# Kernel optimization log

Measured on AMD Instinct MI355X. Metric: run time of the kernel, lower is better.

## Reference

```python
import jax, jax.numpy as jnp
import numpy as np

IO, H, S, N = 64, 1024, 512, 64

def setup_inputs() -> dict:
    key = jax.random.key(0)
    ks = jax.random.split(key, 6)
    scale = 0.05  # keep activations in a sane range for tanh/softmax
    return {
        "states": jax.random.normal(ks[0], (N, S, H), jnp.float32) * scale,
        "output_set": jax.random.normal(ks[1], (IO, H), jnp.float32) * scale,
        "Wo": jax.random.normal(ks[2], (2 * H, H), jnp.float32) * scale,
        "bo": jax.random.normal(ks[3], (H,), jnp.float32) * scale,
        "Wc": jax.random.normal(ks[4], (IO * H, IO), jnp.float32) * scale,
        "bc": jax.random.normal(ks[5], (IO,), jnp.float32) * scale,
    }

def reference(states, output_set, Wo, bo, Wc, bc):
    # Batched over the n_states Python loop of the original module.
    # attn scores: output_set [io,h] x states [n,s,h] -> [n,io,s]
    attn = jnp.einsum('ih,nsh->nis', output_set, states)
    attn = jax.nn.softmax(attn, axis=-1)  # softmax over context (sm_over_context=True)
    mix = jnp.einsum('nis,nsh->nih', attn, states)            # [n,io,h]
    out = jnp.broadcast_to(output_set[None], mix.shape)       # [n,io,h]
    combined = jnp.concatenate([mix, out], axis=-1)           # [n,io,2h]
    o = combined @ Wo + bo                                    # linear_out: 2h -> h
    logits = jnp.tanh(o).reshape(o.shape[0], -1) @ Wc + bc    # C: io*h -> io
    return logits
```

## Files before the change

### kernel.cpp

```cpp
#include <hip/hip_runtime.h>
#include <hip/hip_bf16.h>

#define IOdim 64
#define Hdim  1024
#define Sdim  512
#define Nbat  64

typedef __bf16 bf16x8_t __attribute__((ext_vector_type(8)));
typedef float  f32x4_t  __attribute__((ext_vector_type(4)));

#define MFMA16(a, b, c) __builtin_amdgcn_mfma_f32_16x16x32_bf16((a), (b), (c), 0, 0, 0)

__device__ __forceinline__ unsigned short f2bf(float f) {
    return __builtin_bit_cast(unsigned short, (__bf16)f);
}
__device__ __forceinline__ bf16x8_t cvt8(float4 p0, float4 p1) {
    bf16x8_t b;
    b[0] = (__bf16)p0.x; b[1] = (__bf16)p0.y; b[2] = (__bf16)p0.z; b[3] = (__bf16)p0.w;
    b[4] = (__bf16)p1.x; b[5] = (__bf16)p1.y; b[6] = (__bf16)p1.z; b[7] = (__bf16)p1.w;
    return b;
}

__global__ __launch_bounds__(256) void cvt_kernel(const float* __restrict__ in,
                                                  unsigned short* __restrict__ outp,
                                                  int nElem) {
    int idx = blockIdx.x * 256 + threadIdx.x;
    if (idx < nElem) outp[idx] = f2bf(in[idx]);
}

__global__ __launch_bounds__(256) void transpose_cvt(const float* __restrict__ in,
                                                     unsigned short* __restrict__ outp,
                                                     int R, int C) {
    __shared__ float tile[32][33];
    int c0 = blockIdx.x * 32, r0 = blockIdx.y * 32;
    int tx = threadIdx.x, ty = threadIdx.y;
#pragma unroll
    for (int i = 0; i < 4; i++) {
        int r = ty + i * 8;
        tile[r][tx] = in[(size_t)(r0 + r) * C + c0 + tx];
    }
    __syncthreads();
#pragma unroll
    for (int i = 0; i < 4; i++) {
        int r = ty + i * 8;
        outp[(size_t)(c0 + r) * R + r0 + tx] = f2bf(tile[tx][r]);
    }
}

__global__ __launch_bounds__(256) void scores_kernel(const float* __restrict__ states,
                                                     const unsigned short* __restrict__ osb,
                                                     float* __restrict__ attnf) {
    int n = blockIdx.y;
    int tid = threadIdx.x, lane = tid & 63, g = tid >> 6;
    int col = lane & 15, quad = lane >> 4;
    int s = blockIdx.x * 64 + g * 16 + col;
    const float* srow = states + (size_t)(n * Sdim + s) * Hdim + quad * 8;
    const unsigned short* ap = osb + (size_t)col * Hdim + quad * 8;
    f32x4_t acc0 = {0,0,0,0}, acc1 = {0,0,0,0}, acc2 = {0,0,0,0}, acc3 = {0,0,0,0};
    for (int kc = 0; kc < Hdim; kc += 32) {
        float4 p0 = *(const float4*)(srow + kc);
        float4 p1 = *(const float4*)(srow + kc + 4);
        bf16x8_t b  = cvt8(p0, p1);
        bf16x8_t a0 = *(const bf16x8_t*)(ap + kc);
        bf16x8_t a1 = *(const bf16x8_t*)(ap + 16 * Hdim + kc);
        bf16x8_t a2 = *(const bf16x8_t*)(ap + 32 * Hdim + kc);
        bf16x8_t a3 = *(const bf16x8_t*)(ap + 48 * Hdim + kc);
        acc0 = MFMA16(a0, b, acc0);
        acc1 = MFMA16(a1, b, acc1);
        acc2 = MFMA16(a2, b, acc2);
        acc3 = MFMA16(a3, b, acc3);
    }
    f32x4_t accs[4] = {acc0, acc1, acc2, acc3};
    float* ob = attnf + (size_t)(n * IOdim) * Sdim + blockIdx.x * 64 + g * 16 + col;
#pragma unroll
    for (int ai = 0; ai < 4; ai++)
#pragma unroll
        for (int r = 0; r < 4; r++) {
            int i = ai * 16 + quad * 4 + r;
            ob[i * Sdim] = accs[ai][r];
        }
}

__global__ __launch_bounds__(256) void softmax_kernel(const float* __restrict__ attnf,
                                                      unsigned short* __restrict__ attnb) {
    int row = blockIdx.x * 4 + (threadIdx.x >> 6);
    int lane = threadIdx.x & 63;
    const float* p = attnf + (size_t)row * Sdim + lane * 8;
    float4 v0 = ((const float4*)p)[0];
    float4 v1 = ((const float4*)p)[1];
    float v[8] = {v0.x, v0.y, v0.z, v0.w, v1.x, v1.y, v1.z, v1.w};
    float m = v[0];
#pragma unroll
    for (int j = 1; j < 8; j++) m = fmaxf(m, v[j]);
#pragma unroll
    for (int off = 32; off > 0; off >>= 1) m = fmaxf(m, __shfl_xor(m, off));
    float sum = 0.f;
#pragma unroll
    for (int j = 0; j < 8; j++) { v[j] = __expf(v[j] - m); sum += v[j]; }
#pragma unroll
    for (int off = 32; off > 0; off >>= 1) sum += __shfl_xor(sum, off);
    float inv = 1.0f / sum;
    union { unsigned short u[8]; uint4 q; } res;
#pragma unroll
    for (int j = 0; j < 8; j++) res.u[j] = f2bf(v[j] * inv);
    *(uint4*)(attnb + (size_t)row * Sdim + lane * 8) = res.q;
}

__global__ __launch_bounds__(256) void mix_kernel(const float* __restrict__ states,
                                                  const unsigned short* __restrict__ attnb,
                                                  unsigned short* __restrict__ mixb) {
    __shared__ unsigned short Tlds[64 * 72];
    int n = blockIdx.y, h0 = blockIdx.x * 64;
    int tid = threadIdx.x, lane = tid & 63, g = tid >> 6;
    int col = lane & 15, quad = lane >> 4;
    f32x4_t acc0 = {0,0,0,0}, acc1 = {0,0,0,0}, acc2 = {0,0,0,0}, acc3 = {0,0,0,0};
    const unsigned short* ap = attnb + (size_t)(n * IOdim + col) * Sdim + quad * 8;
    for (int sc = 0; sc < Sdim; sc += 64) {
        union { unsigned short u[16]; uint4 q[2]; } pk;
        const float* sp = states + (size_t)(n * Sdim + sc + g * 16) * Hdim + h0 + lane;
#pragma unroll
        for (int rep = 0; rep < 16; rep++) pk.u[rep] = f2bf(sp[(size_t)rep * Hdim]);
        if (sc) __syncthreads();
        *(uint4*)(Tlds + lane * 72 + g * 16)     = pk.q[0];
        *(uint4*)(Tlds + lane * 72 + g * 16 + 8) = pk.q[1];
        __syncthreads();
#pragma unroll
        for (int ks = 0; ks < 64; ks += 32) {
            bf16x8_t b  = *(const bf16x8_t*)(Tlds + (g * 16 + col) * 72 + ks + quad * 8);
            bf16x8_t a0 = *(const bf16x8_t*)(ap + sc + ks);
            bf16x8_t a1 = *(const bf16x8_t*)(ap + 16 * Sdim + sc + ks);
            bf16x8_t a2 = *(const bf16x8_t*)(ap + 32 * Sdim + sc + ks);
            bf16x8_t a3 = *(const bf16x8_t*)(ap + 48 * Sdim + sc + ks);
            acc0 = MFMA16(a0, b, acc0);
            acc1 = MFMA16(a1, b, acc1);
            acc2 = MFMA16(a2, b, acc2);
            acc3 = MFMA16(a3, b, acc3);
        }
    }
    f32x4_t accs[4] = {acc0, acc1, acc2, acc3};
    int h = h0 + g * 16 + col;
#pragma unroll
    for (int ai = 0; ai < 4; ai++)
#pragma unroll
        for (int r = 0; r < 4; r++) {
            int i = ai * 16 + quad * 4 + r;
            mixb[(size_t)(n * IOdim + i) * Hdim + h] = f2bf(accs[ai][r]);
        }
}

__global__ __launch_bounds__(256) void out_gemm(const unsigned short* __restrict__ mixb,
                                                const unsigned short* __restrict__ osb,
                                                const unsigned short* __restrict__ woT,
                                                const float* __restrict__ bo,
                                                unsigned short* __restrict__ tb) {
    int h0 = blockIdx.x * 128, r0 = blockIdx.y * 64;
    int tid = threadIdx.x, lane = tid & 63, g = tid >> 6;
    int col = lane & 15, quad = lane >> 4;
    f32x4_t accA0 = {0,0,0,0}, accA1 = {0,0,0,0}, accA2 = {0,0,0,0}, accA3 = {0,0,0,0};
    f32x4_t accB0 = {0,0,0,0}, accB1 = {0,0,0,0}, accB2 = {0,0,0,0}, accB3 = {0,0,0,0};
    int h1 = h0 + g * 16 + col, h2 = h1 + 64;
    const unsigned short* brow0 = woT + (size_t)h1 * 2048 + quad * 8;
    const unsigned short* brow1 = woT + (size_t)h2 * 2048 + quad * 8;
    const unsigned short* am = mixb + (size_t)(r0 + col) * Hdim + quad * 8;
    const unsigned short* ao = osb + (size_t)col * Hdim + quad * 8;
    for (int kc = 0; kc < 2048; kc += 32) {
        const unsigned short* abase = (kc < 1024) ? (am + kc) : (ao + (kc - 1024));
        bf16x8_t a0 = *(const bf16x8_t*)(abase);
        bf16x8_t a1 = *(const bf16x8_t*)(abase + 16 * Hdim);
        bf16x8_t a2 = *(const bf16x8_t*)(abase + 32 * Hdim);
        bf16x8_t a3 = *(const bf16x8_t*)(abase + 48 * Hdim);
        bf16x8_t b0 = *(const bf16x8_t*)(brow0 + kc);
        bf16x8_t b1 = *(const bf16x8_t*)(brow1 + kc);
        accA0 = MFMA16(a0, b0, accA0);
        accA1 = MFMA16(a1, b0, accA1);
        accA2 = MFMA16(a2, b0, accA2);
        accA3 = MFMA16(a3, b0, accA3);
        accB0 = MFMA16(a0, b1, accB0);
        accB1 = MFMA16(a1, b1, accB1);
        accB2 = MFMA16(a2, b1, accB2);
        accB3 = MFMA16(a3, b1, accB3);
    }
    f32x4_t accsA[4] = {accA0, accA1, accA2, accA3};
    f32x4_t accsB[4] = {accB0, accB1, accB2, accB3};
    float bo1 = bo[h1], bo2 = bo[h2];
#pragma unroll
    for (int ai = 0; ai < 4; ai++)
#pragma unroll
        for (int r = 0; r < 4; r++) {
            int rr = r0 + ai * 16 + quad * 4 + r;
            tb[(size_t)rr * Hdim + h1] = f2bf(tanhf(accsA[ai][r] + bo1));
            tb[(size_t)rr * Hdim + h2] = f2bf(tanhf(accsB[ai][r] + bo2));
        }
}

__global__ __launch_bounds__(256) void final_gemm(const unsigned short* __restrict__ tb,
                                                  const unsigned short* __restrict__ wcT,
                                                  float* __restrict__ partials) {
    int kc0 = blockIdx.x * 256;
    int tid = threadIdx.x, lane = tid & 63, g = tid >> 6;
    int col = lane & 15, quad = lane >> 4;
    f32x4_t acc0 = {0,0,0,0}, acc1 = {0,0,0,0}, acc2 = {0,0,0,0}, acc3 = {0,0,0,0};
    const unsigned short* ap = tb + (size_t)col * 65536 + kc0 + quad * 8;
    const unsigned short* bp = wcT + (size_t)(g * 16 + col) * 65536 + kc0 + quad * 8;
    for (int kc = 0; kc < 256; kc += 32) {
        bf16x8_t b  = *(const bf16x8_t*)(bp + kc);
        bf16x8_t a0 = *(const bf16x8_t*)(ap + kc);
        bf16x8_t a1 = *(const bf16x8_t*)(ap + (size_t)16 * 65536 + kc);
        bf16x8_t a2 = *(const bf16x8_t*)(ap + (size_t)32 * 65536 + kc);
        bf16x8_t a3 = *(const bf16x8_t*)(ap + (size_t)48 * 65536 + kc);
        acc0 = MFMA16(a0, b, acc0);
        acc1 = MFMA16(a1, b, acc1);
        acc2 = MFMA16(a2, b, acc2);
        acc3 = MFMA16(a3, b, acc3);
    }
    f32x4_t accs[4] = {acc0, acc1, acc2, acc3};
    int j = g * 16 + col;
    float* pb = partials + blockIdx.x * 4096;
#pragma unroll
    for (int ai = 0; ai < 4; ai++)
#pragma unroll
        for (int r = 0; r < 4; r++) {
            int nn = ai * 16 + quad * 4 + r;
            pb[nn * 64 + j] = accs[ai][r];
        }
}

__global__ __launch_bounds__(256) void reduce_kernel(const float* __restrict__ partials,
                                                     const float* __restrict__ bc,
                                                     float* __restrict__ out) {
    int idx = blockIdx.x * 256 + threadIdx.x;
    float s = bc[idx & 63];
#pragma unroll 8
    for (int b = 0; b < 256; b++) s += partials[b * 4096 + idx];
    out[idx] = s;
}

extern "C" void kernel_launch(void* const* d_in, const int* in_sizes, int n_in,
                              void* d_out, int out_size, void* d_ws, size_t ws_size,
                              hipStream_t stream) {
    const float* states     = (const float*)d_in[0];
    const float* output_set = (const float*)d_in[1];
    const float* Wo         = (const float*)d_in[2];
    const float* bo         = (const float*)d_in[3];
    const float* Wc         = (const float*)d_in[4];
    const float* bc         = (const float*)d_in[5];
    float* out = (float*)d_out;

    char* ws = (char*)d_ws;
    float*          attnf = (float*)ws;
    unsigned short* attnb = (unsigned short*)(ws + (8u  << 20));
    unsigned short* mixb  = (unsigned short*)(ws + (12u << 20));
    unsigned short* tb    = (unsigned short*)(ws + (20u << 20));
    unsigned short* woT   = (unsigned short*)(ws + (28u << 20));
    unsigned short* osb   = (unsigned short*)(ws + (32u << 20));
    unsigned short* wcT   = (unsigned short*)(ws + (32u << 20) + (1u << 18));
    float*          parts = (float*)(ws + (41u << 20));

    cvt_kernel<<<dim3(IOdim * Hdim / 256), dim3(256), 0, stream>>>(output_set, osb, IOdim * Hdim);
    transpose_cvt<<<dim3(Hdim / 32, 2048 / 32), dim3(32, 8), 0, stream>>>(Wo, woT, 2048, Hdim);
    transpose_cvt<<<dim3(64 / 32, 65536 / 32), dim3(32, 8), 0, stream>>>(Wc, wcT, 65536, 64);
    scores_kernel<<<dim3(Sdim / 64, Nbat), dim3(256), 0, stream>>>(states, osb, attnf);
    softmax_kernel<<<dim3(Nbat * IOdim / 4), dim3(256), 0, stream>>>(attnf, attnb);
    mix_kernel<<<dim3(Hdim / 64, Nbat), dim3(256), 0, stream>>>(states, attnb, mixb);
    out_gemm<<<dim3(Hdim / 128, Nbat * IOdim / 64), dim3(256), 0, stream>>>(mixb, osb, woT, bo, tb);
    final_gemm<<<dim3(256), dim3(256), 0, stream>>>(tb, wcT, parts);
    reduce_kernel<<<dim3(16), dim3(256), 0, stream>>>(parts, bc, out);
}
```

Measured before the change: 381.6 us.

## Software-prefetch GEMM loops and retile out_gemm with LDS async loads

```diff
diff --git a/kernel.cpp b/kernel.cpp
--- a/kernel.cpp
+++ b/kernel.cpp
@@ -19,6 +19,11 @@
     b[0] = (__bf16)p0.x; b[1] = (__bf16)p0.y; b[2] = (__bf16)p0.z; b[3] = (__bf16)p0.w;
     b[4] = (__bf16)p1.x; b[5] = (__bf16)p1.y; b[6] = (__bf16)p1.z; b[7] = (__bf16)p1.w;
     return b;
+}
+__device__ __forceinline__ void async16(const void* g, void* l) {
+    __builtin_amdgcn_global_load_lds(
+        (const __attribute__((address_space(1))) void*)g,
+        (__attribute__((address_space(3))) void*)l, 16, 0, 0);
 }
 
 __global__ __launch_bounds__(256) void cvt_kernel(const float* __restrict__ in,
@@ -57,18 +62,34 @@
     const float* srow = states + (size_t)(n * Sdim + s) * Hdim + quad * 8;
     const unsigned short* ap = osb + (size_t)col * Hdim + quad * 8;
     f32x4_t acc0 = {0,0,0,0}, acc1 = {0,0,0,0}, acc2 = {0,0,0,0}, acc3 = {0,0,0,0};
-    for (int kc = 0; kc < Hdim; kc += 32) {
-        float4 p0 = *(const float4*)(srow + kc);
-        float4 p1 = *(const float4*)(srow + kc + 4);
-        bf16x8_t b  = cvt8(p0, p1);
-        bf16x8_t a0 = *(const bf16x8_t*)(ap + kc);
-        bf16x8_t a1 = *(const bf16x8_t*)(ap + 16 * Hdim + kc);
-        bf16x8_t a2 = *(const bf16x8_t*)(ap + 32 * Hdim + kc);
-        bf16x8_t a3 = *(const bf16x8_t*)(ap + 48 * Hdim + kc);
-        acc0 = MFMA16(a0, b, acc0);
-        acc1 = MFMA16(a1, b, acc1);
-        acc2 = MFMA16(a2, b, acc2);
-        acc3 = MFMA16(a3, b, acc3);
+    float4 c0 = *(const float4*)(srow);
+    float4 c1 = *(const float4*)(srow + 4);
+    bf16x8_t A0 = *(const bf16x8_t*)(ap);
+    bf16x8_t A1 = *(const bf16x8_t*)(ap + 16 * Hdim);
+    bf16x8_t A2 = *(const bf16x8_t*)(ap + 32 * Hdim);
+    bf16x8_t A3 = *(const bf16x8_t*)(ap + 48 * Hdim);
+#pragma unroll 4
+    for (int kc = 0; kc < Hdim - 32; kc += 32) {
+        int kn = kc + 32;
+        float4 n0 = *(const float4*)(srow + kn);
+        float4 n1 = *(const float4*)(srow + kn + 4);
+        bf16x8_t N0 = *(const bf16x8_t*)(ap + kn);
+        bf16x8_t N1 = *(const bf16x8_t*)(ap + 16 * Hdim + kn);
+        bf16x8_t N2 = *(const bf16x8_t*)(ap + 32 * Hdim + kn);
+        bf16x8_t N3 = *(const bf16x8_t*)(ap + 48 * Hdim + kn);
+        bf16x8_t b = cvt8(c0, c1);
+        acc0 = MFMA16(A0, b, acc0);
+        acc1 = MFMA16(A1, b, acc1);
+        acc2 = MFMA16(A2, b, acc2);
+        acc3 = MFMA16(A3, b, acc3);
+        c0 = n0; c1 = n1; A0 = N0; A1 = N1; A2 = N2; A3 = N3;
+    }
+    {
+        bf16x8_t b = cvt8(c0, c1);
+        acc0 = MFMA16(A0, b, acc0);
+        acc1 = MFMA16(A1, b, acc1);
+        acc2 = MFMA16(A2, b, acc2);
+        acc3 = MFMA16(A3, b, acc3);
     }
     f32x4_t accs[4] = {acc0, acc1, acc2, acc3};
     float* ob = attnf + (size_t)(n * IOdim) * Sdim + blockIdx.x * 64 + g * 16 + col;
@@ -115,14 +136,22 @@
     int col = lane & 15, quad = lane >> 4;
     f32x4_t acc0 = {0,0,0,0}, acc1 = {0,0,0,0}, acc2 = {0,0,0,0}, acc3 = {0,0,0,0};
     const unsigned short* ap = attnb + (size_t)(n * IOdim + col) * Sdim + quad * 8;
+    const float* sbase = states + (size_t)n * Sdim * Hdim + h0 + lane;
+    float cur[16];
+#pragma unroll
+    for (int rep = 0; rep < 16; rep++) cur[rep] = sbase[(size_t)(g * 16 + rep) * Hdim];
     for (int sc = 0; sc < Sdim; sc += 64) {
         union { unsigned short u[16]; uint4 q[2]; } pk;
-        const float* sp = states + (size_t)(n * Sdim + sc + g * 16) * Hdim + h0 + lane;
-#pragma unroll
-        for (int rep = 0; rep < 16; rep++) pk.u[rep] = f2bf(sp[(size_t)rep * Hdim]);
+#pragma unroll
+        for (int rep = 0; rep < 16; rep++) pk.u[rep] = f2bf(cur[rep]);
         if (sc) __syncthreads();
         *(uint4*)(Tlds + lane * 72 + g * 16)     = pk.q[0];
         *(uint4*)(Tlds + lane * 72 + g * 16 + 8) = pk.q[1];
+        if (sc + 64 < Sdim) {
+#pragma unroll
+            for (int rep = 0; rep < 16; rep++)
+                cur[rep] = sbase[(size_t)(sc + 64 + g * 16 + rep) * Hdim];
+        }
         __syncthreads();
 #pragma unroll
         for (int ks = 0; ks < 64; ks += 32) {
@@ -153,44 +182,60 @@
                                                 const unsigned short* __restrict__ woT,
                                                 const float* __restrict__ bo,
                                                 unsigned short* __restrict__ tb) {
-    int h0 = blockIdx.x * 128, r0 = blockIdx.y * 64;
-    int tid = threadIdx.x, lane = tid & 63, g = tid >> 6;
+    __shared__ unsigned short Ald[128 * 32];
+    __shared__ unsigned short Bld[128 * 32];
+    int h0 = blockIdx.x * 128, r0 = blockIdx.y * 128;
+    int tid = threadIdx.x, lane = tid & 63, w = tid >> 6;
     int col = lane & 15, quad = lane >> 4;
-    f32x4_t accA0 = {0,0,0,0}, accA1 = {0,0,0,0}, accA2 = {0,0,0,0}, accA3 = {0,0,0,0};
-    f32x4_t accB0 = {0,0,0,0}, accB1 = {0,0,0,0}, accB2 = {0,0,0,0}, accB3 = {0,0,0,0};
-    int h1 = h0 + g * 16 + col, h2 = h1 + 64;
-    const unsigned short* brow0 = woT + (size_t)h1 * 2048 + quad * 8;
-    const unsigned short* brow1 = woT + (size_t)h2 * 2048 + quad * 8;
-    const unsigned short* am = mixb + (size_t)(r0 + col) * Hdim + quad * 8;
-    const unsigned short* ao = osb + (size_t)col * Hdim + quad * 8;
+    int wx = w & 1, wy = w >> 1;
+    int rowA = tid >> 2, seg = tid & 3;
+    f32x4_t acc[4][4] = {};
+    const unsigned short* m1 = mixb + (size_t)(r0 + rowA) * Hdim + seg * 8;
+    const unsigned short* m2 = mixb + (size_t)(r0 + rowA + 64) * Hdim + seg * 8;
+    const unsigned short* o1 = osb + (size_t)rowA * Hdim + seg * 8;
+    const unsigned short* w1 = woT + (size_t)(h0 + rowA) * 2048 + seg * 8;
+    const unsigned short* w2 = woT + (size_t)(h0 + rowA + 64) * 2048 + seg * 8;
+    unsigned short* lA1 = Ald + (size_t)tid * 8;
+    unsigned short* lA2 = Ald + (size_t)(tid + 256) * 8;
+    unsigned short* lB1 = Bld + (size_t)tid * 8;
+    unsigned short* lB2 = Bld + (size_t)(tid + 256) * 8;
     for (int kc = 0; kc < 2048; kc += 32) {
-        const unsigned short* abase = (kc < 1024) ? (am + kc) : (ao + (kc - 1024));
-        bf16x8_t a0 = *(const bf16x8_t*)(abase);
-        bf16x8_t a1 = *(const bf16x8_t*)(abase + 16 * Hdim);
-        bf16x8_t a2 = *(const bf16x8_t*)(abase + 32 * Hdim);
-        bf16x8_t a3 = *(const bf16x8_t*)(abase + 48 * Hdim);
-        bf16x8_t b0 = *(const bf16x8_t*)(brow0 + kc);
-        bf16x8_t b1 = *(const bf16x8_t*)(brow1 + kc);
-        accA0 = MFMA16(a0, b0, accA0);
-        accA1 = MFMA16(a1, b0, accA1);
-        accA2 = MFMA16(a2, b0, accA2);
-        accA3 = MFMA16(a3, b0, accA3);
-        accB0 = MFMA16(a0, b1, accB0);
-        accB1 = MFMA16(a1, b1, accB1);
-        accB2 = MFMA16(a2, b1, accB2);
-        accB3 = MFMA16(a3, b1, accB3);
-    }
-    f32x4_t accsA[4] = {accA0, accA1, accA2, accA3};
-    f32x4_t accsB[4] = {accB0, accB1, accB2, accB3};
-    float bo1 = bo[h1], bo2 = bo[h2];
-#pragma unroll
-    for (int ai = 0; ai < 4; ai++)
-#pragma unroll
-        for (int r = 0; r < 4; r++) {
-            int rr = r0 + ai * 16 + quad * 4 + r;
-            tb[(size_t)rr * Hdim + h1] = f2bf(tanhf(accsA[ai][r] + bo1));
-            tb[(size_t)rr * Hdim + h2] = f2bf(tanhf(accsB[ai][r] + bo2));
-        }
+        if (kc < 1024) {
+            async16(m1 + kc, lA1);
+            async16(m2 + kc, lA2);
+        } else {
+            async16(o1 + (kc - 1024), lA1);
+            async16(o1 + (kc - 1024), lA2);
+        }
+        async16(w1 + kc, lB1);
+        async16(w2 + kc, lB2);
+        __syncthreads();
+        bf16x8_t af[4], bfr[4];
+#pragma unroll
+        for (int mi = 0; mi < 4; mi++)
+            af[mi] = *(const bf16x8_t*)(Ald + (wy * 64 + mi * 16 + col) * 32 + quad * 8);
+#pragma unroll
+        for (int ni = 0; ni < 4; ni++)
+            bfr[ni] = *(const bf16x8_t*)(Bld + (wx * 64 + ni * 16 + col) * 32 + quad * 8);
+#pragma unroll
+        for (int mi = 0; mi < 4; mi++)
+#pragma unroll
+            for (int ni = 0; ni < 4; ni++)
+                acc[mi][ni] = MFMA16(af[mi], bfr[ni], acc[mi][ni]);
+        __syncthreads();
+    }
+#pragma unroll
+    for (int ni = 0; ni < 4; ni++) {
+        int h = h0 + wx * 64 + ni * 16 + col;
+        float bov = bo[h];
+#pragma unroll
+        for (int mi = 0; mi < 4; mi++)
+#pragma unroll
+            for (int r = 0; r < 4; r++) {
+                int rr = r0 + wy * 64 + mi * 16 + quad * 4 + r;
+                tb[(size_t)rr * Hdim + h] = f2bf(tanhf(acc[mi][ni][r] + bov));
+            }
+    }
 }
 
 __global__ __launch_bounds__(256) void final_gemm(const unsigned short* __restrict__ tb,
@@ -202,17 +247,29 @@
     f32x4_t acc0 = {0,0,0,0}, acc1 = {0,0,0,0}, acc2 = {0,0,0,0}, acc3 = {0,0,0,0};
     const unsigned short* ap = tb + (size_t)col * 65536 + kc0 + quad * 8;
     const unsigned short* bp = wcT + (size_t)(g * 16 + col) * 65536 + kc0 + quad * 8;
-    for (int kc = 0; kc < 256; kc += 32) {
-        bf16x8_t b  = *(const bf16x8_t*)(bp + kc);
-        bf16x8_t a0 = *(const bf16x8_t*)(ap + kc);
-        bf16x8_t a1 = *(const bf16x8_t*)(ap + (size_t)16 * 65536 + kc);
-        bf16x8_t a2 = *(const bf16x8_t*)(ap + (size_t)32 * 65536 + kc);
-        bf16x8_t a3 = *(const bf16x8_t*)(ap + (size_t)48 * 65536 + kc);
-        acc0 = MFMA16(a0, b, acc0);
-        acc1 = MFMA16(a1, b, acc1);
-        acc2 = MFMA16(a2, b, acc2);
-        acc3 = MFMA16(a3, b, acc3);
-    }
+    bf16x8_t B  = *(const bf16x8_t*)(bp);
+    bf16x8_t A0 = *(const bf16x8_t*)(ap);
+    bf16x8_t A1 = *(const bf16x8_t*)(ap + (size_t)16 * 65536);
+    bf16x8_t A2 = *(const bf16x8_t*)(ap + (size_t)32 * 65536);
+    bf16x8_t A3 = *(const bf16x8_t*)(ap + (size_t)48 * 65536);
+#pragma unroll
+    for (int kc = 0; kc < 256 - 32; kc += 32) {
+        int kn = kc + 32;
+        bf16x8_t Bn  = *(const bf16x8_t*)(bp + kn);
+        bf16x8_t N0 = *(const bf16x8_t*)(ap + kn);
+        bf16x8_t N1 = *(const bf16x8_t*)(ap + (size_t)16 * 65536 + kn);
+        bf16x8_t N2 = *(const bf16x8_t*)(ap + (size_t)32 * 65536 + kn);
+        bf16x8_t N3 = *(const bf16x8_t*)(ap + (size_t)48 * 65536 + kn);
+        acc0 = MFMA16(A0, B, acc0);
+        acc1 = MFMA16(A1, B, acc1);
+        acc2 = MFMA16(A2, B, acc2);
+        acc3 = MFMA16(A3, B, acc3);
+        B = Bn; A0 = N0; A1 = N1; A2 = N2; A3 = N3;
+    }
+    acc0 = MFMA16(A0, B, acc0);
+    acc1 = MFMA16(A1, B, acc1);
+    acc2 = MFMA16(A2, B, acc2);
+    acc3 = MFMA16(A3, B, acc3);
     f32x4_t accs[4] = {acc0, acc1, acc2, acc3};
     int j = g * 16 + col;
     float* pb = partials + blockIdx.x * 4096;
@@ -262,7 +319,7 @@
     scores_kernel<<<dim3(Sdim / 64, Nbat), dim3(256), 0, stream>>>(states, osb, attnf);
     softmax_kernel<<<dim3(Nbat * IOdim / 4), dim3(256), 0, stream>>>(attnf, attnb);
     mix_kernel<<<dim3(Hdim / 64, Nbat), dim3(256), 0, stream>>>(states, attnb, mixb);
-    out_gemm<<<dim3(Hdim / 128, Nbat * IOdim / 64), dim3(256), 0, stream>>>(mixb, osb, woT, bo, tb);
+    out_gemm<<<dim3(Hdim / 128, Nbat * IOdim / 128), dim3(256), 0, stream>>>(mixb, osb, woT, bo, tb);
     final_gemm<<<dim3(256), dim3(256), 0, stream>>>(tb, wcT, parts);
     reduce_kernel<<<dim3(16), dim3(256), 0, stream>>>(parts, bc, out);
 }
```

After: 344.5 us. 1.11x faster.
